# Optimization experiments

Measured on AMD Instinct MI355X. Metric: run time of the kernel, lower is better.

## Reference

```python
import jax, jax.numpy as jnp
import numpy as np

N_NODES = 1_000_000
N_EDGES = 32_000_000
NUM_HOP = 3


def setup_inputs() -> dict:
    key = jax.random.key(0)
    k1, k2 = jax.random.split(key)
    h = jnp.ones((N_NODES, 1), dtype=jnp.float32)  # graph.ndata['one']
    src = jax.random.randint(k1, (N_EDGES,), 0, N_NODES, dtype=jnp.int64 if jax.config.read('jax_enable_x64') else jnp.int32)
    dst = jax.random.randint(k2, (N_EDGES,), 0, N_NODES, dtype=jnp.int64 if jax.config.read('jax_enable_x64') else jnp.int32)
    # SAGEConv weights, init to ones per reset_parameters(); bias=False
    w_self = jnp.ones((NUM_HOP, 1, 1), dtype=jnp.float32)
    w_neigh = jnp.ones((NUM_HOP, 1, 1), dtype=jnp.float32)
    return {"h": h, "src": src, "dst": dst, "w_self": w_self, "w_neigh": w_neigh}


def reference(h, src, dst, w_self, w_neigh):
    # Stacked SAGEConv(aggregator='add', bias=False, feat_drop=0):
    #   h_out = h @ W_self + segment_sum(h[src] -> dst) @ W_neigh
    # dropout p=0 between layers is identity.
    n = h.shape[0]
    num_hop = w_self.shape[0]
    for i in range(num_hop):
        neigh = jax.ops.segment_sum(h[src], dst, num_segments=n)  # [N, F] sum over in-edges
        h = h @ w_self[i] + neigh @ w_neigh[i]
    return h
```

## Files before the change

kernel.cpp:

```cpp
#include <hip/hip_runtime.h>


constexpr int BLK     = 256;
constexpr int BBITS   = 12;
constexpr int BUCKET  = 1 << BBITS;
constexpr int NB_MAX  = 256;
constexpr int SPLIT   = 8;
constexpr int TILE    = 8192;
constexpr int HBLOCKS = 1024;


__global__ void zero_u32(unsigned* __restrict__ p, int n) {
    int i = blockIdx.x * blockDim.x + threadIdx.x;
    if (i < n) p[i] = 0u;
}

__global__ void hist_kernel(const int* __restrict__ dst, int ne,
                            unsigned* __restrict__ count, int nb) {
    __shared__ unsigned hist[NB_MAX];
    for (int b = threadIdx.x; b < NB_MAX; b += blockDim.x) hist[b] = 0u;
    __syncthreads();
    const int4* dst4 = reinterpret_cast<const int4*>(dst);
    int nvec = ne >> 2;
    for (int i = blockIdx.x * blockDim.x + threadIdx.x; i < nvec;
         i += gridDim.x * blockDim.x) {
        int4 d = dst4[i];
        atomicAdd(&hist[d.x >> BBITS], 1u);
        atomicAdd(&hist[d.y >> BBITS], 1u);
        atomicAdd(&hist[d.z >> BBITS], 1u);
        atomicAdd(&hist[d.w >> BBITS], 1u);
    }
    if (blockIdx.x == 0 && threadIdx.x == 0)
        for (int i = nvec << 2; i < ne; ++i) atomicAdd(&hist[dst[i] >> BBITS], 1u);
    __syncthreads();
    for (int b = threadIdx.x; b < nb; b += blockDim.x)
        if (hist[b]) atomicAdd(&count[b], hist[b]);
}

__global__ void scan_kernel(const unsigned* __restrict__ count,
                            unsigned* __restrict__ offsets,
                            unsigned* __restrict__ cursor, int nb) {
    __shared__ unsigned s[NB_MAX];
    int t = threadIdx.x;
    unsigned v = (t < nb) ? count[t] : 0u;
    s[t] = v;
    __syncthreads();
    for (int d = 1; d < NB_MAX; d <<= 1) {
        unsigned u = (t >= d) ? s[t - d] : 0u;
        __syncthreads();
        s[t] += u;
        __syncthreads();
    }
    unsigned excl = s[t] - v;
    if (t < nb) { offsets[t] = excl; cursor[t] = excl; }
    if (t == nb - 1) offsets[nb] = excl + v;
}

__global__ __launch_bounds__(256)
void bin_kernel(const int* __restrict__ src, const int* __restrict__ dst, int ne,
                unsigned* __restrict__ cursor, unsigned* __restrict__ recs) {
    __shared__ unsigned hist[NB_MAX];
    __shared__ unsigned start[NB_MAX];
    __shared__ unsigned lpos[NB_MAX];
    __shared__ unsigned gbase[NB_MAX];
    __shared__ unsigned rec[TILE];
    __shared__ unsigned char bid[TILE];

    int base = blockIdx.x * TILE;
    int cnt = min(TILE, ne - base);
    if (cnt <= 0) return;

    for (int b = threadIdx.x; b < NB_MAX; b += blockDim.x) hist[b] = 0u;
    __syncthreads();

    int nvec = cnt & ~3;
    const int4* dst4 = reinterpret_cast<const int4*>(dst + base);
    const int4* src4 = reinterpret_cast<const int4*>(src + base);

    for (int i = threadIdx.x; i < (nvec >> 2); i += blockDim.x) {
        int4 d = dst4[i];
        atomicAdd(&hist[d.x >> BBITS], 1u);
        atomicAdd(&hist[d.y >> BBITS], 1u);
        atomicAdd(&hist[d.z >> BBITS], 1u);
        atomicAdd(&hist[d.w >> BBITS], 1u);
    }
    if (threadIdx.x == 0)
        for (int i = nvec; i < cnt; ++i) atomicAdd(&hist[dst[base + i] >> BBITS], 1u);
    __syncthreads();

    {
        int t = threadIdx.x;
        unsigned v = hist[t];
        start[t] = v;
        __syncthreads();
        for (int d = 1; d < NB_MAX; d <<= 1) {
            unsigned u = (t >= d) ? start[t - d] : 0u;
            __syncthreads();
            start[t] += u;
            __syncthreads();
        }
        unsigned excl = start[t] - v;
        __syncthreads();
        start[t] = excl;
        lpos[t]  = excl;
        if (v) gbase[t] = atomicAdd(&cursor[t], v);
        __syncthreads();
    }

    for (int i = threadIdx.x; i < (nvec >> 2); i += blockDim.x) {
        int4 d = dst4[i];
        int4 s = src4[i];
        int dd[4] = {d.x, d.y, d.z, d.w};
        int ss[4] = {s.x, s.y, s.z, s.w};
#pragma unroll
        for (int k = 0; k < 4; ++k) {
            int b = dd[k] >> BBITS;
            unsigned p = atomicAdd(&lpos[b], 1u);
            rec[p] = ((unsigned)(dd[k] & (BUCKET - 1)) << 20) | (unsigned)ss[k];
            bid[p] = (unsigned char)b;
        }
    }
    if (threadIdx.x == 0)
        for (int i = nvec; i < cnt; ++i) {
            int dd = dst[base + i], ss = src[base + i];
            int b = dd >> BBITS;
            unsigned p = atomicAdd(&lpos[b], 1u);
            rec[p] = ((unsigned)(dd & (BUCKET - 1)) << 20) | (unsigned)ss;
            bid[p] = (unsigned char)b;
        }
    __syncthreads();

    for (int i = threadIdx.x; i < cnt; i += blockDim.x) {
        int b = bid[i];
        recs[gbase[b] + ((unsigned)i - start[b])] = rec[i];
    }
}

__global__ __launch_bounds__(256)
void agg_kernel(const float* __restrict__ curh,
                const unsigned* __restrict__ recs,
                const unsigned* __restrict__ offsets,
                float* __restrict__ partials) {
    __shared__ float acc[BUCKET];
    int b = blockIdx.x / SPLIT;
    int s = blockIdx.x % SPLIT;
    for (int i = threadIdx.x; i < BUCKET; i += blockDim.x) acc[i] = 0.0f;
    __syncthreads();
    unsigned bs = offsets[b], be = offsets[b + 1];
    unsigned cnt = be - bs;
    unsigned per = (cnt + SPLIT - 1) / SPLIT;
    unsigned ss = bs + (unsigned)s * per;
    unsigned se = min(ss + per, be);
    for (unsigned i = ss + threadIdx.x; i < se; i += blockDim.x) {
        unsigned r = recs[i];
        float v = curh[r & 0xFFFFFu];
        atomicAdd(&acc[r >> 20], v);
    }
    __syncthreads();
    float* out = partials + ((size_t)blockIdx.x) * BUCKET;
    for (int i = threadIdx.x; i < BUCKET; i += blockDim.x) out[i] = acc[i];
}

__global__ void reduce_combine(const float* __restrict__ curh,
                               const float* __restrict__ partials,
                               const float* __restrict__ w_self,
                               const float* __restrict__ w_neigh, int hop,
                               float* __restrict__ out, int n) {
    int i = blockIdx.x * blockDim.x + threadIdx.x;
    if (i >= n) return;
    int b = i >> BBITS, l = i & (BUCKET - 1);
    const float* p = partials + ((size_t)b * SPLIT) * BUCKET + l;
    float sum = 0.0f;
#pragma unroll
    for (int s = 0; s < SPLIT; ++s) sum += p[(size_t)s * BUCKET];
    out[i] = curh[i] * w_self[hop] + sum * w_neigh[hop];
}


__global__ void zero_f32(float* __restrict__ p, int n) {
    int i = blockIdx.x * blockDim.x + threadIdx.x;
    if (i < n) p[i] = 0.0f;
}

__global__ void scatter_add(const float* __restrict__ h, const int* __restrict__ src,
                            const int* __restrict__ dst, float* __restrict__ neigh, int ne) {
    int i = blockIdx.x * blockDim.x + threadIdx.x;
    int base = i * 4;
    if (base + 3 < ne) {
        int4 s = *reinterpret_cast<const int4*>(src + base);
        int4 d = *reinterpret_cast<const int4*>(dst + base);
        atomicAdd(&neigh[d.x], h[s.x]);
        atomicAdd(&neigh[d.y], h[s.y]);
        atomicAdd(&neigh[d.z], h[s.z]);
        atomicAdd(&neigh[d.w], h[s.w]);
    } else if (base < ne) {
        for (int e = base; e < ne; ++e) atomicAdd(&neigh[dst[e]], h[src[e]]);
    }
}

__global__ void combine(const float* __restrict__ h, const float* __restrict__ neigh,
                        const float* __restrict__ w_self, const float* __restrict__ w_neigh,
                        int hop, float* __restrict__ out, int n) {
    int i = blockIdx.x * blockDim.x + threadIdx.x;
    if (i < n) out[i] = h[i] * w_self[hop] + neigh[i] * w_neigh[hop];
}


extern "C" void kernel_launch(void* const* d_in, const int* in_sizes, int n_in,
                              void* d_out, int out_size, void* d_ws, size_t ws_size,
                              hipStream_t stream) {
    const float* h       = (const float*)d_in[0];
    const int*   src     = (const int*)d_in[1];
    const int*   dst     = (const int*)d_in[2];
    const float* w_self  = (const float*)d_in[3];
    const float* w_neigh = (const float*)d_in[4];
    float* out = (float*)d_out;

    const int n    = in_sizes[0];
    const int ne   = in_sizes[1];
    const int hops = in_sizes[3];

    const int nb = (n + BUCKET - 1) >> BBITS;

    size_t off = 0;
    auto take = [&](size_t bytes) { size_t o = off; off = (off + bytes + 255) & ~255UL; return o; };
    size_t o_recs     = take((size_t)ne * 4);
    size_t o_count    = take((size_t)NB_MAX * 4);
    size_t o_offsets  = take((size_t)(NB_MAX + 1) * 4);
    size_t o_cursor   = take((size_t)NB_MAX * 4);
    size_t o_partials = take((size_t)nb * SPLIT * BUCKET * 4);
    size_t o_buf      = take((size_t)n * 4);
    size_t needed = off;

    char* ws = (char*)d_ws;
    bool fast = (ws_size >= needed) && (nb <= NB_MAX) && (n <= (1 << 20));

    if (fast) {
        unsigned* recs     = (unsigned*)(ws + o_recs);
        unsigned* count    = (unsigned*)(ws + o_count);
        unsigned* offsets  = (unsigned*)(ws + o_offsets);
        unsigned* cursor   = (unsigned*)(ws + o_cursor);
        float*    partials = (float*)(ws + o_partials);
        float*    buf      = (float*)(ws + o_buf);

        zero_u32<<<1, NB_MAX, 0, stream>>>(count, NB_MAX);
        hist_kernel<<<HBLOCKS, BLK, 0, stream>>>(dst, ne, count, nb);
        scan_kernel<<<1, NB_MAX, 0, stream>>>(count, offsets, cursor, nb);
        bin_kernel<<<(ne + TILE - 1) / TILE, BLK, 0, stream>>>(src, dst, ne, cursor, recs);

        const int gridN = (n + BLK - 1) / BLK;
        const float* cur = h;
        for (int hop = 0; hop < hops; ++hop) {
            float* nxt = (hop == hops - 1) ? out : buf;
            agg_kernel<<<nb * SPLIT, BLK, 0, stream>>>(cur, recs, offsets, partials);
            reduce_combine<<<gridN, BLK, 0, stream>>>(cur, partials, w_self, w_neigh, hop, nxt, n);
            cur = nxt;
        }
    } else {
        float* buf   = (float*)d_ws;
        float* neigh = buf + n;
        const int gridN = (n + BLK - 1) / BLK;
        const int gridE = ((ne + 3) / 4 + BLK - 1) / BLK;
        const float* cur = h;
        for (int hop = 0; hop < hops; ++hop) {
            float* nxt = (hop == hops - 1) ? out : buf;
            zero_f32<<<gridN, BLK, 0, stream>>>(neigh, n);
            scatter_add<<<gridE, BLK, 0, stream>>>(cur, src, dst, neigh, ne);
            combine<<<gridN, BLK, 0, stream>>>(cur, neigh, w_self, w_neigh, hop, nxt, n);
            cur = nxt;
        }
    }
}
```

Measured before the change: 987.1 us.

## Vectorize aggregation with padded buckets, 1024-thread blocks, and two-way split

Bucket offsets are padded to multiples of 4 so the aggregation kernel can read records as 16-byte nontemporal vectors. It runs 1024-thread blocks with only two splits per bucket, which shrinks the partials buffer and lets reduce_combine process four nodes per thread with vector loads. The global histogram spreads each block's shared counters across 4 sub-slots to reduce atomic contention. Input streams use nontemporal loads and stores. Fewer blocks per bucket lowers parallelism, and with 1024 threads each block shares one 4096-entry accumulator, which may raise LDS atomic contention.

After: 935.5 us. 1.06x faster.

```diff
diff --git a/kernel.cpp b/kernel.cpp
--- a/kernel.cpp
+++ b/kernel.cpp
@@ -1,11 +1,14 @@
 #include <hip/hip_runtime.h>
 
+
+typedef unsigned u32x4 __attribute__((ext_vector_type(4)));
+typedef float    f32x4 __attribute__((ext_vector_type(4)));
 
 constexpr int BLK     = 256;
 constexpr int BBITS   = 12;
 constexpr int BUCKET  = 1 << BBITS;
 constexpr int NB_MAX  = 256;
-constexpr int SPLIT   = 8;
+constexpr int SPLIT   = 2;
 constexpr int TILE    = 8192;
 constexpr int HBLOCKS = 1024;
 
@@ -17,24 +20,28 @@
 
 __global__ void hist_kernel(const int* __restrict__ dst, int ne,
                             unsigned* __restrict__ count, int nb) {
-    __shared__ unsigned hist[NB_MAX];
-    for (int b = threadIdx.x; b < NB_MAX; b += blockDim.x) hist[b] = 0u;
-    __syncthreads();
-    const int4* dst4 = reinterpret_cast<const int4*>(dst);
+    __shared__ unsigned hist[NB_MAX * 4];
+    for (int b = threadIdx.x; b < NB_MAX * 4; b += blockDim.x) hist[b] = 0u;
+    __syncthreads();
+    const u32x4* dst4 = reinterpret_cast<const u32x4*>(dst);
     int nvec = ne >> 2;
+    int sub = threadIdx.x & 3;
     for (int i = blockIdx.x * blockDim.x + threadIdx.x; i < nvec;
          i += gridDim.x * blockDim.x) {
-        int4 d = dst4[i];
-        atomicAdd(&hist[d.x >> BBITS], 1u);
-        atomicAdd(&hist[d.y >> BBITS], 1u);
-        atomicAdd(&hist[d.z >> BBITS], 1u);
-        atomicAdd(&hist[d.w >> BBITS], 1u);
+        u32x4 d = __builtin_nontemporal_load(dst4 + i);
+        atomicAdd(&hist[((d.x >> BBITS) << 2) | sub], 1u);
+        atomicAdd(&hist[((d.y >> BBITS) << 2) | sub], 1u);
+        atomicAdd(&hist[((d.z >> BBITS) << 2) | sub], 1u);
+        atomicAdd(&hist[((d.w >> BBITS) << 2) | sub], 1u);
     }
     if (blockIdx.x == 0 && threadIdx.x == 0)
-        for (int i = nvec << 2; i < ne; ++i) atomicAdd(&hist[dst[i] >> BBITS], 1u);
-    __syncthreads();
-    for (int b = threadIdx.x; b < nb; b += blockDim.x)
-        if (hist[b]) atomicAdd(&count[b], hist[b]);
+        for (int i = nvec << 2; i < ne; ++i)
+            atomicAdd(&hist[(((unsigned)dst[i] >> BBITS) << 2)], 1u);
+    __syncthreads();
+    for (int b = threadIdx.x; b < nb; b += blockDim.x) {
+        unsigned v = hist[b * 4] + hist[b * 4 + 1] + hist[b * 4 + 2] + hist[b * 4 + 3];
+        if (v) atomicAdd(&count[b], v);
+    }
 }
 
 __global__ void scan_kernel(const unsigned* __restrict__ count,
@@ -42,8 +49,9 @@
                             unsigned* __restrict__ cursor, int nb) {
     __shared__ unsigned s[NB_MAX];
     int t = threadIdx.x;
-    unsigned v = (t < nb) ? count[t] : 0u;
-    s[t] = v;
+    unsigned v  = (t < nb) ? count[t] : 0u;
+    unsigned pv = (v + 3u) & ~3u;
+    s[t] = pv;
     __syncthreads();
     for (int d = 1; d < NB_MAX; d <<= 1) {
         unsigned u = (t >= d) ? s[t - d] : 0u;
@@ -51,9 +59,8 @@
         s[t] += u;
         __syncthreads();
     }
-    unsigned excl = s[t] - v;
+    unsigned excl = s[t] - pv;
     if (t < nb) { offsets[t] = excl; cursor[t] = excl; }
-    if (t == nb - 1) offsets[nb] = excl + v;
 }
 
 __global__ __launch_bounds__(256)
@@ -74,18 +81,19 @@
     __syncthreads();
 
     int nvec = cnt & ~3;
-    const int4* dst4 = reinterpret_cast<const int4*>(dst + base);
-    const int4* src4 = reinterpret_cast<const int4*>(src + base);
+    const u32x4* dst4 = reinterpret_cast<const u32x4*>(dst + base);
+    const u32x4* src4 = reinterpret_cast<const u32x4*>(src + base);
 
     for (int i = threadIdx.x; i < (nvec >> 2); i += blockDim.x) {
-        int4 d = dst4[i];
+        u32x4 d = dst4[i];
         atomicAdd(&hist[d.x >> BBITS], 1u);
         atomicAdd(&hist[d.y >> BBITS], 1u);
         atomicAdd(&hist[d.z >> BBITS], 1u);
         atomicAdd(&hist[d.w >> BBITS], 1u);
     }
     if (threadIdx.x == 0)
-        for (int i = nvec; i < cnt; ++i) atomicAdd(&hist[dst[base + i] >> BBITS], 1u);
+        for (int i = nvec; i < cnt; ++i)
+            atomicAdd(&hist[(unsigned)dst[base + i] >> BBITS], 1u);
     __syncthreads();
 
     {
@@ -108,24 +116,24 @@
     }
 
     for (int i = threadIdx.x; i < (nvec >> 2); i += blockDim.x) {
-        int4 d = dst4[i];
-        int4 s = src4[i];
-        int dd[4] = {d.x, d.y, d.z, d.w};
-        int ss[4] = {s.x, s.y, s.z, s.w};
+        u32x4 d = __builtin_nontemporal_load(dst4 + i);
+        u32x4 s = __builtin_nontemporal_load(src4 + i);
+        unsigned dd[4] = {d.x, d.y, d.z, d.w};
+        unsigned ss[4] = {s.x, s.y, s.z, s.w};
 #pragma unroll
         for (int k = 0; k < 4; ++k) {
-            int b = dd[k] >> BBITS;
+            unsigned b = dd[k] >> BBITS;
             unsigned p = atomicAdd(&lpos[b], 1u);
-            rec[p] = ((unsigned)(dd[k] & (BUCKET - 1)) << 20) | (unsigned)ss[k];
+            rec[p] = ((dd[k] & (BUCKET - 1)) << 20) | ss[k];
             bid[p] = (unsigned char)b;
         }
     }
     if (threadIdx.x == 0)
         for (int i = nvec; i < cnt; ++i) {
-            int dd = dst[base + i], ss = src[base + i];
-            int b = dd >> BBITS;
+            unsigned dd = (unsigned)dst[base + i], ss = (unsigned)src[base + i];
+            unsigned b = dd >> BBITS;
             unsigned p = atomicAdd(&lpos[b], 1u);
-            rec[p] = ((unsigned)(dd & (BUCKET - 1)) << 20) | (unsigned)ss;
+            rec[p] = ((dd & (BUCKET - 1)) << 20) | ss;
             bid[p] = (unsigned char)b;
         }
     __syncthreads();
@@ -136,29 +144,45 @@
     }
 }
 
-__global__ __launch_bounds__(256)
+__global__ __launch_bounds__(1024, 8)
 void agg_kernel(const float* __restrict__ curh,
                 const unsigned* __restrict__ recs,
                 const unsigned* __restrict__ offsets,
+                const unsigned* __restrict__ count,
                 float* __restrict__ partials) {
     __shared__ float acc[BUCKET];
-    int b = blockIdx.x / SPLIT;
-    int s = blockIdx.x % SPLIT;
-    for (int i = threadIdx.x; i < BUCKET; i += blockDim.x) acc[i] = 0.0f;
-    __syncthreads();
-    unsigned bs = offsets[b], be = offsets[b + 1];
-    unsigned cnt = be - bs;
-    unsigned per = (cnt + SPLIT - 1) / SPLIT;
-    unsigned ss = bs + (unsigned)s * per;
-    unsigned se = min(ss + per, be);
-    for (unsigned i = ss + threadIdx.x; i < se; i += blockDim.x) {
-        unsigned r = recs[i];
-        float v = curh[r & 0xFFFFFu];
-        atomicAdd(&acc[r >> 20], v);
-    }
-    __syncthreads();
-    float* out = partials + ((size_t)blockIdx.x) * BUCKET;
-    for (int i = threadIdx.x; i < BUCKET; i += blockDim.x) out[i] = acc[i];
+    int b = blockIdx.x >> 1;
+    int s = blockIdx.x & 1;
+    for (int i = threadIdx.x; i < BUCKET; i += 1024) acc[i] = 0.0f;
+    __syncthreads();
+    unsigned bs  = offsets[b];
+    unsigned cnt = count[b];
+    unsigned half = (cnt >> 1) & ~3u;
+    unsigned ss = bs + (s ? half : 0u);
+    unsigned sc = s ? (cnt - half) : half;
+    unsigned n4 = sc >> 2;
+    const u32x4* rq = reinterpret_cast<const u32x4*>(recs + ss);
+    for (unsigned q = threadIdx.x; q < n4; q += 1024) {
+        u32x4 r = __builtin_nontemporal_load(rq + q);
+        float v0 = curh[r.x & 0xFFFFFu];
+        float v1 = curh[r.y & 0xFFFFFu];
+        float v2 = curh[r.z & 0xFFFFFu];
+        float v3 = curh[r.w & 0xFFFFFu];
+        atomicAdd(&acc[r.x >> 20], v0);
+        atomicAdd(&acc[r.y >> 20], v1);
+        atomicAdd(&acc[r.z >> 20], v2);
+        atomicAdd(&acc[r.w >> 20], v3);
+    }
+    unsigned tb = ss + (n4 << 2);
+    unsigned rem = sc & 3u;
+    if (threadIdx.x < rem) {
+        unsigned r = recs[tb + threadIdx.x];
+        atomicAdd(&acc[r >> 20], curh[r & 0xFFFFFu]);
+    }
+    __syncthreads();
+    float* outp = partials + ((size_t)blockIdx.x) * BUCKET;
+    for (int i = threadIdx.x; i < BUCKET; i += 1024)
+        __builtin_nontemporal_store(acc[i], outp + i);
 }
 
 __global__ void reduce_combine(const float* __restrict__ curh,
@@ -167,13 +191,26 @@
                                const float* __restrict__ w_neigh, int hop,
                                float* __restrict__ out, int n) {
     int i = blockIdx.x * blockDim.x + threadIdx.x;
-    if (i >= n) return;
-    int b = i >> BBITS, l = i & (BUCKET - 1);
-    const float* p = partials + ((size_t)b * SPLIT) * BUCKET + l;
-    float sum = 0.0f;
-#pragma unroll
-    for (int s = 0; s < SPLIT; ++s) sum += p[(size_t)s * BUCKET];
-    out[i] = curh[i] * w_self[hop] + sum * w_neigh[hop];
+    int nq = (n + 3) >> 2;
+    if (i >= nq) return;
+    int node = i << 2;
+    float wsv = w_self[hop], wnv = w_neigh[hop];
+    int b = node >> BBITS, l = node & (BUCKET - 1);
+    const float* p0 = partials + ((size_t)b * SPLIT) * BUCKET + l;
+    const float* p1 = p0 + BUCKET;
+    if (node + 3 < n) {
+        f32x4 a = __builtin_nontemporal_load(reinterpret_cast<const f32x4*>(p0));
+        f32x4 c = __builtin_nontemporal_load(reinterpret_cast<const f32x4*>(p1));
+        f32x4 hh = *reinterpret_cast<const f32x4*>(curh + node);
+        f32x4 o = hh * wsv + (a + c) * wnv;
+        *reinterpret_cast<f32x4*>(out + node) = o;
+    } else {
+        for (int j = node; j < n; ++j) {
+            int bb = j >> BBITS, ll = j & (BUCKET - 1);
+            const float* pp = partials + ((size_t)bb * SPLIT) * BUCKET + ll;
+            out[j] = curh[j] * wsv + (pp[0] + pp[BUCKET]) * wnv;
+        }
+    }
 }
 
 
@@ -224,9 +261,9 @@
 
     size_t off = 0;
     auto take = [&](size_t bytes) { size_t o = off; off = (off + bytes + 255) & ~255UL; return o; };
-    size_t o_recs     = take((size_t)ne * 4);
+    size_t o_recs     = take(((size_t)ne + 4 * NB_MAX) * 4);
     size_t o_count    = take((size_t)NB_MAX * 4);
-    size_t o_offsets  = take((size_t)(NB_MAX + 1) * 4);
+    size_t o_offsets  = take((size_t)NB_MAX * 4);
     size_t o_cursor   = take((size_t)NB_MAX * 4);
     size_t o_partials = take((size_t)nb * SPLIT * BUCKET * 4);
     size_t o_buf      = take((size_t)n * 4);
@@ -248,12 +285,13 @@
         scan_kernel<<<1, NB_MAX, 0, stream>>>(count, offsets, cursor, nb);
         bin_kernel<<<(ne + TILE - 1) / TILE, BLK, 0, stream>>>(src, dst, ne, cursor, recs);
 
-        const int gridN = (n + BLK - 1) / BLK;
+        const int nq = (n + 3) >> 2;
+        const int gridQ = (nq + BLK - 1) / BLK;
         const float* cur = h;
         for (int hop = 0; hop < hops; ++hop) {
             float* nxt = (hop == hops - 1) ? out : buf;
-            agg_kernel<<<nb * SPLIT, BLK, 0, stream>>>(cur, recs, offsets, partials);
-            reduce_combine<<<gridN, BLK, 0, stream>>>(cur, partials, w_self, w_neigh, hop, nxt, n);
+            agg_kernel<<<nb * SPLIT, 1024, 0, stream>>>(cur, recs, offsets, count, partials);
+            reduce_combine<<<gridQ, BLK, 0, stream>>>(cur, partials, w_self, w_neigh, hop, nxt, n);
             cur = nxt;
         }
     } else {
```
